# Kernel tuning notes

Hardware: AMD Instinct MI355X
Metric: run time of the kernel (lower is better)

Reference implementation:

```python
import jax, jax.numpy as jnp
import numpy as np

HIDDEN, FFN, N_EXPERTS, TOP_K = 1024, 4096, 8, 2


def setup_inputs() -> dict:
    key = jax.random.key(0)
    ks = jax.random.split(key, 8)
    s_h = 1.0 / np.sqrt(HIDDEN)
    s_f = 1.0 / np.sqrt(FFN)
    return {
        "x": jax.random.normal(ks[0], (1, 1024, HIDDEN), dtype=jnp.float32),
        "gate_w": jax.random.normal(ks[1], (N_EXPERTS, HIDDEN), dtype=jnp.float32) * s_h,
        "gate_b": jnp.zeros((N_EXPERTS,), dtype=jnp.float32),
        "w1": jax.random.normal(ks[2], (N_EXPERTS, HIDDEN, FFN), dtype=jnp.float32) * s_h,
        "b1": jnp.zeros((N_EXPERTS, FFN), dtype=jnp.float32),
        "w2": jax.random.normal(ks[3], (N_EXPERTS, FFN, HIDDEN), dtype=jnp.float32) * s_f,
        "b2": jnp.zeros((N_EXPERTS, HIDDEN), dtype=jnp.float32),
    }


def reference(x, gate_w, gate_b, w1, b1, w2, b2):
    B, S, H = x.shape
    x_flat = x.reshape(-1, H)  # (T, H)
    # Router: top-k gating with softmax over selected logits
    logits = x_flat @ gate_w.T + gate_b  # (T, E)
    top_w, sel = jax.lax.top_k(logits, TOP_K)  # (T, K)
    rw = jax.nn.softmax(top_w, axis=-1)  # (T, K)
    # combine[t, e] = router weight of expert e for token t (0 if not selected)
    combine = jnp.sum(jax.nn.one_hot(sel, N_EXPERTS, dtype=x.dtype) * rw[..., None], axis=1)  # (T, E)
    # Dense all-expert FFN, combined with routing weights (zero weight => zero contribution,
    # identical math to the masked gather/scatter loop in the torch module)
    h = jax.nn.gelu(jnp.einsum('th,ehf->tef', x_flat, w1) + b1, approximate=False)  # (T, E, F)
    y = jnp.einsum('tef,efh->teh', h, w2) + b2  # (T, E, H)
    out = jnp.einsum('te,teh->th', combine, y)  # (T, H)
    return out.reshape(B, S, H)
```

## Files before the change

### kernel.cpp

```cpp
#include <hip/hip_runtime.h>


typedef __bf16 bf16;
typedef __bf16 bf16x8 __attribute__((ext_vector_type(8)));
typedef float floatx4 __attribute__((ext_vector_type(4)));

#define T_TOK 1024
#define HID 1024
#define FFN 4096
#define NEXP 8
#define BM 128
#define BN 128
#define BK 32
#define LP 36

__global__ void xconv_k(const float* __restrict__ x, bf16* __restrict__ xb) {
  int i = blockIdx.x * 256 + threadIdx.x;
  float4 a = ((const float4*)x)[i * 2];
  float4 b = ((const float4*)x)[i * 2 + 1];
  bf16 t[8] = {(bf16)a.x, (bf16)a.y, (bf16)a.z, (bf16)a.w,
               (bf16)b.x, (bf16)b.y, (bf16)b.z, (bf16)b.w};
  *(bf16x8*)&xb[(size_t)i * 8] = *(bf16x8*)t;
}

__global__ void router_k(const float* __restrict__ x, const float* __restrict__ gw,
                         const float* __restrict__ gb, int* __restrict__ cnt,
                         int* __restrict__ elist, float* __restrict__ ewt) {
  int wave = threadIdx.x >> 6;
  int lane = threadIdx.x & 63;
  int t = blockIdx.x * 4 + wave;
  const float* xr = x + (size_t)t * HID;
  float xv[16];
#pragma unroll
  for (int j = 0; j < 16; j++) xv[j] = xr[lane + 64 * j];
  float logits[NEXP];
#pragma unroll
  for (int e = 0; e < NEXP; e++) {
    const float* g = gw + (size_t)e * HID;
    float s = 0.f;
#pragma unroll
    for (int j = 0; j < 16; j++) s += xv[j] * g[lane + 64 * j];
#pragma unroll
    for (int off = 32; off; off >>= 1) s += __shfl_xor(s, off, 64);
    logits[e] = s + gb[e];
  }
  int i0 = 0; float l0 = logits[0];
#pragma unroll
  for (int e = 1; e < NEXP; e++) if (logits[e] > l0) { l0 = logits[e]; i0 = e; }
  int i1 = -1; float l1 = -3.0e38f;
#pragma unroll
  for (int e = 0; e < NEXP; e++) if (e != i0 && logits[e] > l1) { l1 = logits[e]; i1 = e; }
  if (lane == 0) {
    float w0 = 1.f / (1.f + expf(l1 - l0));
    float w1 = 1.f - w0;
    int p0 = atomicAdd(cnt + i0, 1);
    elist[i0 * T_TOK + p0] = t * 2 + 0; ewt[i0 * T_TOK + p0] = w0;
    int p1 = atomicAdd(cnt + i1, 1);
    elist[i1 * T_TOK + p1] = t * 2 + 1; ewt[i1 * T_TOK + p1] = w1;
  }
}

__global__ __launch_bounds__(256)
void gemm1_k(const bf16* __restrict__ xb, const float* __restrict__ w1,
             const float* __restrict__ b1, const int* __restrict__ cnt,
             const int* __restrict__ elist, bf16* __restrict__ hbuf) {
  int e = blockIdx.z;
  int c = cnt[e];
  int m0 = blockIdx.y * BM;
  if (m0 >= c) return;
  int n0 = blockIdx.x * BN;

  __shared__ __align__(16) bf16 As[BM][LP];
  __shared__ __align__(16) bf16 Bs[BN][LP];

  int tid = threadIdx.x;
  int ar = tid >> 1;
  int ac = (tid & 1) * 16;
  int ra = m0 + ar; if (ra >= c) ra = c - 1;
  const bf16* aptr = xb + (size_t)(elist[e * T_TOK + ra] >> 1) * HID + ac;
  int bn = tid & 127;
  int bk = (tid >> 7) * 16;
  const float* bptr = w1 + (size_t)e * HID * FFN + (size_t)bk * FFN + n0 + bn;

  uint4 a0, a1;
  float bfl[16];
  a0 = *(const uint4*)(aptr);
  a1 = *(const uint4*)(aptr + 8);
#pragma unroll
  for (int j = 0; j < 16; j++) bfl[j] = bptr[(size_t)j * FFN];

  floatx4 acc[4][4] = {};
  int ln = tid & 63, wv = tid >> 6;
  int fm = ln & 15, quad = ln >> 4;
  int wm = (wv & 1) * 64, wn = (wv >> 1) * 64;

  for (int t = 0; t < HID / BK; t++) {
    bf16 bb[16];
#pragma unroll
    for (int j = 0; j < 16; j++) bb[j] = (bf16)bfl[j];
    uint4 wa0 = a0, wa1 = a1;
    __syncthreads();
    *(uint4*)&As[ar][ac]      = wa0;
    *(uint4*)&As[ar][ac + 8]  = wa1;
    *(bf16x8*)&Bs[bn][bk]     = *(bf16x8*)&bb[0];
    *(bf16x8*)&Bs[bn][bk + 8] = *(bf16x8*)&bb[8];
    if (t + 1 < HID / BK) {
      aptr += BK;
      a0 = *(const uint4*)(aptr);
      a1 = *(const uint4*)(aptr + 8);
      bptr += (size_t)BK * FFN;
#pragma unroll
      for (int j = 0; j < 16; j++) bfl[j] = bptr[(size_t)j * FFN];
    }
    __syncthreads();
    bf16x8 af[4], bfr[4];
#pragma unroll
    for (int i = 0; i < 4; i++) af[i] = *(const bf16x8*)&As[wm + i * 16 + fm][quad * 8];
#pragma unroll
    for (int j = 0; j < 4; j++) bfr[j] = *(const bf16x8*)&Bs[wn + j * 16 + fm][quad * 8];
#pragma unroll
    for (int i = 0; i < 4; i++)
#pragma unroll
      for (int j = 0; j < 4; j++)
        acc[i][j] = __builtin_amdgcn_mfma_f32_16x16x32_bf16(af[i], bfr[j], acc[i][j], 0, 0, 0);
  }

  const float* b1e = b1 + (size_t)e * FFN;
#pragma unroll
  for (int i = 0; i < 4; i++) {
    int rb = m0 + wm + i * 16 + quad * 4;
#pragma unroll
    for (int j = 0; j < 4; j++) {
      int col = n0 + wn + j * 16 + fm;
      float bias = b1e[col];
#pragma unroll
      for (int r = 0; r < 4; r++) {
        int row = rb + r;
        if (row < c) {
          int slot = elist[e * T_TOK + row];
          float v = acc[i][j][r] + bias;
          float g = 0.5f * v * (1.f + erff(v * 0.70710678118654752f));
          hbuf[(size_t)slot * FFN + col] = (bf16)g;
        }
      }
    }
  }
}

__global__ __launch_bounds__(256)
void gemm2_k(const bf16* __restrict__ hbuf, const float* __restrict__ w2,
             const float* __restrict__ b2, const int* __restrict__ cnt,
             const int* __restrict__ elist, const float* __restrict__ ewt,
             float* __restrict__ part) {
  int e = blockIdx.z & 7;
  int ks = blockIdx.z >> 3;
  int c = cnt[e];
  int m0 = blockIdx.y * BM;
  if (m0 >= c) return;
  int n0 = blockIdx.x * BN;
  int kbeg = ks * (FFN / 4);

  __shared__ __align__(16) bf16 As[BM][LP];
  __shared__ __align__(16) bf16 Bs[BN][LP];

  int tid = threadIdx.x;
  int ar = tid >> 1;
  int ac = (tid & 1) * 16;
  int ra = m0 + ar; if (ra >= c) ra = c - 1;
  const bf16* aptr = hbuf + (size_t)elist[e * T_TOK + ra] * FFN + kbeg + ac;
  int bn = tid & 127;
  int bk = (tid >> 7) * 16;
  const float* bptr = w2 + (size_t)e * FFN * HID + (size_t)(kbeg + bk) * HID + n0 + bn;

  uint4 a0, a1;
  float bfl[16];
  a0 = *(const uint4*)(aptr);
  a1 = *(const uint4*)(aptr + 8);
#pragma unroll
  for (int j = 0; j < 16; j++) bfl[j] = bptr[(size_t)j * HID];

  floatx4 acc[4][4] = {};
  int ln = tid & 63, wv = tid >> 6;
  int fm = ln & 15, quad = ln >> 4;
  int wm = (wv & 1) * 64, wn = (wv >> 1) * 64;

  const int NT = (FFN / 4) / BK;
  for (int t = 0; t < NT; t++) {
    bf16 bb[16];
#pragma unroll
    for (int j = 0; j < 16; j++) bb[j] = (bf16)bfl[j];
    uint4 wa0 = a0, wa1 = a1;
    __syncthreads();
    *(uint4*)&As[ar][ac]      = wa0;
    *(uint4*)&As[ar][ac + 8]  = wa1;
    *(bf16x8*)&Bs[bn][bk]     = *(bf16x8*)&bb[0];
    *(bf16x8*)&Bs[bn][bk + 8] = *(bf16x8*)&bb[8];
    if (t + 1 < NT) {
      aptr += BK;
      a0 = *(const uint4*)(aptr);
      a1 = *(const uint4*)(aptr + 8);
      bptr += (size_t)BK * HID;
#pragma unroll
      for (int j = 0; j < 16; j++) bfl[j] = bptr[(size_t)j * HID];
    }
    __syncthreads();
    bf16x8 af[4], bfr[4];
#pragma unroll
    for (int i = 0; i < 4; i++) af[i] = *(const bf16x8*)&As[wm + i * 16 + fm][quad * 8];
#pragma unroll
    for (int j = 0; j < 4; j++) bfr[j] = *(const bf16x8*)&Bs[wn + j * 16 + fm][quad * 8];
#pragma unroll
    for (int i = 0; i < 4; i++)
#pragma unroll
      for (int j = 0; j < 4; j++)
        acc[i][j] = __builtin_amdgcn_mfma_f32_16x16x32_bf16(af[i], bfr[j], acc[i][j], 0, 0, 0);
  }

  const float* b2e = b2 + (size_t)e * HID;
#pragma unroll
  for (int i = 0; i < 4; i++) {
    int rb = m0 + wm + i * 16 + quad * 4;
#pragma unroll
    for (int j = 0; j < 4; j++) {
      int col = n0 + wn + j * 16 + fm;
      float bias = (ks == 0) ? b2e[col] : 0.f;
#pragma unroll
      for (int r = 0; r < 4; r++) {
        int row = rb + r;
        if (row < c) {
          int slot = elist[e * T_TOK + row];
          float w = ewt[e * T_TOK + row];
          part[((size_t)ks * (2 * T_TOK) + slot) * HID + col] = w * (acc[i][j][r] + bias);
        }
      }
    }
  }
}

__global__ void combine_k(const float* __restrict__ part, float* __restrict__ out) {
  int i = blockIdx.x * 256 + threadIdx.x;
  int t = i >> 8;
  int h4 = (i & 255) * 4;
  float4 s = {0.f, 0.f, 0.f, 0.f};
#pragma unroll
  for (int ks = 0; ks < 4; ks++)
#pragma unroll
    for (int sl = 0; sl < 2; sl++) {
      float4 v = *(const float4*)&part[((size_t)ks * (2 * T_TOK) + t * 2 + sl) * HID + h4];
      s.x += v.x; s.y += v.y; s.z += v.z; s.w += v.w;
    }
  *(float4*)&out[(size_t)t * HID + h4] = s;
}

extern "C" void kernel_launch(void* const* d_in, const int* in_sizes, int n_in,
                              void* d_out, int out_size, void* d_ws, size_t ws_size,
                              hipStream_t stream) {
  const float* x  = (const float*)d_in[0];
  const float* gw = (const float*)d_in[1];
  const float* gb = (const float*)d_in[2];
  const float* w1 = (const float*)d_in[3];
  const float* b1 = (const float*)d_in[4];
  const float* w2 = (const float*)d_in[5];
  const float* b2 = (const float*)d_in[6];
  float* out = (float*)d_out;

  char* ws = (char*)d_ws;
  int*   cnt   = (int*)ws;
  int*   elist = (int*)(ws + 1024);
  float* ewt   = (float*)(ws + 1024 + 32768);
  bf16*  xb    = (bf16*)(ws + (1 << 16));
  bf16*  hbuf  = (bf16*)(ws + ((size_t)4 << 20));
  float* part  = (float*)(ws + ((size_t)24 << 20));

  hipMemsetAsync(cnt, 0, 32, stream);
  xconv_k<<<512, 256, 0, stream>>>(x, xb);
  router_k<<<T_TOK / 4, 256, 0, stream>>>(x, gw, gb, cnt, elist, ewt);
  gemm1_k<<<dim3(FFN / BN, 8, NEXP), 256, 0, stream>>>(xb, w1, b1, cnt, elist, hbuf);
  gemm2_k<<<dim3(HID / BN, 8, NEXP * 4), 256, 0, stream>>>(hbuf, w2, b2, cnt, elist, ewt, part);
  combine_k<<<(T_TOK * HID / 4) / 256, 256, 0, stream>>>(part, out);
}
```

Before: 436.2 us.

## Fuse x conversion into router, double-buffer GEMM loads, widen split-K

Folds the fp32-to-bf16 conversion of x into the router kernel and vectorises the router's loads, which removes one launch. Both expert GEMMs now prefetch two K-tiles ahead into register double buffers, load weights as float2 pairs, and pad the LDS rows from 36 to 40 elements. The second GEMM's split-K factor goes from 4 to 8 to put more blocks in flight. The price is more register pressure and twice as many partial buffers for the combine kernel to read.

```diff
diff --git a/kernel.cpp b/kernel.cpp
--- a/kernel.cpp
+++ b/kernel.cpp
@@ -12,34 +12,39 @@
 #define BM 128
 #define BN 128
 #define BK 32
-#define LP 36
-
-__global__ void xconv_k(const float* __restrict__ x, bf16* __restrict__ xb) {
-  int i = blockIdx.x * 256 + threadIdx.x;
-  float4 a = ((const float4*)x)[i * 2];
-  float4 b = ((const float4*)x)[i * 2 + 1];
-  bf16 t[8] = {(bf16)a.x, (bf16)a.y, (bf16)a.z, (bf16)a.w,
-               (bf16)b.x, (bf16)b.y, (bf16)b.z, (bf16)b.w};
-  *(bf16x8*)&xb[(size_t)i * 8] = *(bf16x8*)t;
-}
+#define LP 40
+#define KS2 8
 
 __global__ void router_k(const float* __restrict__ x, const float* __restrict__ gw,
                          const float* __restrict__ gb, int* __restrict__ cnt,
-                         int* __restrict__ elist, float* __restrict__ ewt) {
+                         int* __restrict__ elist, float* __restrict__ ewt,
+                         bf16* __restrict__ xb) {
   int wave = threadIdx.x >> 6;
   int lane = threadIdx.x & 63;
   int t = blockIdx.x * 4 + wave;
-  const float* xr = x + (size_t)t * HID;
-  float xv[16];
-#pragma unroll
-  for (int j = 0; j < 16; j++) xv[j] = xr[lane + 64 * j];
+  const float* xr = x + (size_t)t * HID + lane * 16;
+  float4 xv[4];
+#pragma unroll
+  for (int c = 0; c < 4; c++) xv[c] = ((const float4*)xr)[c];
+  bf16 tv[16];
+#pragma unroll
+  for (int c = 0; c < 4; c++) {
+    tv[c * 4 + 0] = (bf16)xv[c].x; tv[c * 4 + 1] = (bf16)xv[c].y;
+    tv[c * 4 + 2] = (bf16)xv[c].z; tv[c * 4 + 3] = (bf16)xv[c].w;
+  }
+  *(uint4*)&xb[(size_t)t * HID + lane * 16]     = ((uint4*)tv)[0];
+  *(uint4*)&xb[(size_t)t * HID + lane * 16 + 8] = ((uint4*)tv)[1];
+
   float logits[NEXP];
 #pragma unroll
   for (int e = 0; e < NEXP; e++) {
-    const float* g = gw + (size_t)e * HID;
+    const float* g = gw + (size_t)e * HID + lane * 16;
     float s = 0.f;
 #pragma unroll
-    for (int j = 0; j < 16; j++) s += xv[j] * g[lane + 64 * j];
+    for (int c = 0; c < 4; c++) {
+      float4 gv = ((const float4*)g)[c];
+      s += xv[c].x * gv.x + xv[c].y * gv.y + xv[c].z * gv.z + xv[c].w * gv.w;
+    }
 #pragma unroll
     for (int off = 32; off; off >>= 1) s += __shfl_xor(s, off, 64);
     logits[e] = s + gb[e];
@@ -74,56 +79,57 @@
   __shared__ __align__(16) bf16 Bs[BN][LP];
 
   int tid = threadIdx.x;
-  int ar = tid >> 1;
-  int ac = (tid & 1) * 16;
+  int ar = tid >> 1, ah = (tid & 1) * 16;
   int ra = m0 + ar; if (ra >= c) ra = c - 1;
-  const bf16* aptr = xb + (size_t)(elist[e * T_TOK + ra] >> 1) * HID + ac;
-  int bn = tid & 127;
-  int bk = (tid >> 7) * 16;
-  const float* bptr = w1 + (size_t)e * HID * FFN + (size_t)bk * FFN + n0 + bn;
-
-  uint4 a0, a1;
-  float bfl[16];
-  a0 = *(const uint4*)(aptr);
-  a1 = *(const uint4*)(aptr + 8);
-#pragma unroll
-  for (int j = 0; j < 16; j++) bfl[j] = bptr[(size_t)j * FFN];
+  const bf16* abase = xb + (size_t)(elist[e * T_TOK + ra] >> 1) * HID + ah;
+  int bn2 = (tid & 63) * 2;
+  int bq8 = (tid >> 6) * 8;
+  const float* bbase = w1 + (size_t)e * HID * FFN + (size_t)bq8 * FFN + n0 + bn2;
+
+  uint4 pa[2][2];
+  float2 pb[2][8];
+
+#define G1LOAD(s, kt) do { \
+    const bf16* ap = abase + (kt) * BK; \
+    pa[s][0] = *(const uint4*)ap; \
+    pa[s][1] = *(const uint4*)(ap + 8); \
+    const float* bp = bbase + (size_t)(kt) * BK * FFN; \
+    _Pragma("unroll") for (int j = 0; j < 8; j++) \
+      pb[s][j] = *(const float2*)(bp + (size_t)j * FFN); \
+  } while (0)
+
+  G1LOAD(0, 0);
+  G1LOAD(1, 1);
 
   floatx4 acc[4][4] = {};
   int ln = tid & 63, wv = tid >> 6;
   int fm = ln & 15, quad = ln >> 4;
   int wm = (wv & 1) * 64, wn = (wv >> 1) * 64;
-
-  for (int t = 0; t < HID / BK; t++) {
-    bf16 bb[16];
-#pragma unroll
-    for (int j = 0; j < 16; j++) bb[j] = (bf16)bfl[j];
-    uint4 wa0 = a0, wa1 = a1;
-    __syncthreads();
-    *(uint4*)&As[ar][ac]      = wa0;
-    *(uint4*)&As[ar][ac + 8]  = wa1;
-    *(bf16x8*)&Bs[bn][bk]     = *(bf16x8*)&bb[0];
-    *(bf16x8*)&Bs[bn][bk + 8] = *(bf16x8*)&bb[8];
-    if (t + 1 < HID / BK) {
-      aptr += BK;
-      a0 = *(const uint4*)(aptr);
-      a1 = *(const uint4*)(aptr + 8);
-      bptr += (size_t)BK * FFN;
-#pragma unroll
-      for (int j = 0; j < 16; j++) bfl[j] = bptr[(size_t)j * FFN];
-    }
-    __syncthreads();
-    bf16x8 af[4], bfr[4];
-#pragma unroll
-    for (int i = 0; i < 4; i++) af[i] = *(const bf16x8*)&As[wm + i * 16 + fm][quad * 8];
-#pragma unroll
-    for (int j = 0; j < 4; j++) bfr[j] = *(const bf16x8*)&Bs[wn + j * 16 + fm][quad * 8];
-#pragma unroll
-    for (int i = 0; i < 4; i++)
-#pragma unroll
-      for (int j = 0; j < 4; j++)
-        acc[i][j] = __builtin_amdgcn_mfma_f32_16x16x32_bf16(af[i], bfr[j], acc[i][j], 0, 0, 0);
-  }
+  const int NT = HID / BK;
+
+#define G1STEP(s, t) do { \
+    bf16 c0[8], c1[8]; \
+    _Pragma("unroll") for (int j = 0; j < 8; j++) { \
+      c0[j] = (bf16)pb[s][j].x; c1[j] = (bf16)pb[s][j].y; } \
+    uint4 wa0 = pa[s][0], wa1 = pa[s][1]; \
+    __syncthreads(); \
+    *(uint4*)&As[ar][ah]     = wa0; \
+    *(uint4*)&As[ar][ah + 8] = wa1; \
+    *(bf16x8*)&Bs[bn2][bq8]     = *(bf16x8*)c0; \
+    *(bf16x8*)&Bs[bn2 + 1][bq8] = *(bf16x8*)c1; \
+    if ((t) + 2 < NT) G1LOAD(s, (t) + 2); \
+    __syncthreads(); \
+    bf16x8 af[4], bfr[4]; \
+    _Pragma("unroll") for (int i = 0; i < 4; i++) \
+      af[i] = *(const bf16x8*)&As[wm + i * 16 + fm][quad * 8]; \
+    _Pragma("unroll") for (int j = 0; j < 4; j++) \
+      bfr[j] = *(const bf16x8*)&Bs[wn + j * 16 + fm][quad * 8]; \
+    _Pragma("unroll") for (int i = 0; i < 4; i++) \
+      _Pragma("unroll") for (int j = 0; j < 4; j++) \
+        acc[i][j] = __builtin_amdgcn_mfma_f32_16x16x32_bf16(af[i], bfr[j], acc[i][j], 0, 0, 0); \
+  } while (0)
+
+  for (int tt = 0; tt < NT; tt += 2) { G1STEP(0, tt); G1STEP(1, tt + 1); }
 
   const float* b1e = b1 + (size_t)e * FFN;
 #pragma unroll
@@ -158,63 +164,63 @@
   int m0 = blockIdx.y * BM;
   if (m0 >= c) return;
   int n0 = blockIdx.x * BN;
-  int kbeg = ks * (FFN / 4);
+  int kbeg = ks * (FFN / KS2);
 
   __shared__ __align__(16) bf16 As[BM][LP];
   __shared__ __align__(16) bf16 Bs[BN][LP];
 
   int tid = threadIdx.x;
-  int ar = tid >> 1;
-  int ac = (tid & 1) * 16;
+  int ar = tid >> 1, ah = (tid & 1) * 16;
   int ra = m0 + ar; if (ra >= c) ra = c - 1;
-  const bf16* aptr = hbuf + (size_t)elist[e * T_TOK + ra] * FFN + kbeg + ac;
-  int bn = tid & 127;
-  int bk = (tid >> 7) * 16;
-  const float* bptr = w2 + (size_t)e * FFN * HID + (size_t)(kbeg + bk) * HID + n0 + bn;
-
-  uint4 a0, a1;
-  float bfl[16];
-  a0 = *(const uint4*)(aptr);
-  a1 = *(const uint4*)(aptr + 8);
-#pragma unroll
-  for (int j = 0; j < 16; j++) bfl[j] = bptr[(size_t)j * HID];
+  const bf16* abase = hbuf + (size_t)elist[e * T_TOK + ra] * FFN + kbeg + ah;
+  int bn2 = (tid & 63) * 2;
+  int bq8 = (tid >> 6) * 8;
+  const float* bbase = w2 + (size_t)e * FFN * HID + (size_t)(kbeg + bq8) * HID + n0 + bn2;
+
+  uint4 pa[2][2];
+  float2 pb[2][8];
+
+#define G2LOAD(s, kt) do { \
+    const bf16* ap = abase + (kt) * BK; \
+    pa[s][0] = *(const uint4*)ap; \
+    pa[s][1] = *(const uint4*)(ap + 8); \
+    const float* bp = bbase + (size_t)(kt) * BK * HID; \
+    _Pragma("unroll") for (int j = 0; j < 8; j++) \
+      pb[s][j] = *(const float2*)(bp + (size_t)j * HID); \
+  } while (0)
+
+  G2LOAD(0, 0);
+  G2LOAD(1, 1);
 
   floatx4 acc[4][4] = {};
   int ln = tid & 63, wv = tid >> 6;
   int fm = ln & 15, quad = ln >> 4;
   int wm = (wv & 1) * 64, wn = (wv >> 1) * 64;
-
-  const int NT = (FFN / 4) / BK;
-  for (int t = 0; t < NT; t++) {
-    bf16 bb[16];
-#pragma unroll
-    for (int j = 0; j < 16; j++) bb[j] = (bf16)bfl[j];
-    uint4 wa0 = a0, wa1 = a1;
-    __syncthreads();
-    *(uint4*)&As[ar][ac]      = wa0;
-    *(uint4*)&As[ar][ac + 8]  = wa1;
-    *(bf16x8*)&Bs[bn][bk]     = *(bf16x8*)&bb[0];
-    *(bf16x8*)&Bs[bn][bk + 8] = *(bf16x8*)&bb[8];
-    if (t + 1 < NT) {
-      aptr += BK;
-      a0 = *(const uint4*)(aptr);
-      a1 = *(const uint4*)(aptr + 8);
-      bptr += (size_t)BK * HID;
-#pragma unroll
-      for (int j = 0; j < 16; j++) bfl[j] = bptr[(size_t)j * HID];
-    }
-    __syncthreads();
-    bf16x8 af[4], bfr[4];
-#pragma unroll
-    for (int i = 0; i < 4; i++) af[i] = *(const bf16x8*)&As[wm + i * 16 + fm][quad * 8];
-#pragma unroll
-    for (int j = 0; j < 4; j++) bfr[j] = *(const bf16x8*)&Bs[wn + j * 16 + fm][quad * 8];
-#pragma unroll
-    for (int i = 0; i < 4; i++)
-#pragma unroll
-      for (int j = 0; j < 4; j++)
-        acc[i][j] = __builtin_amdgcn_mfma_f32_16x16x32_bf16(af[i], bfr[j], acc[i][j], 0, 0, 0);
-  }
+  const int NT = (FFN / KS2) / BK;
+
+#define G2STEP(s, t) do { \
+    bf16 c0[8], c1[8]; \
+    _Pragma("unroll") for (int j = 0; j < 8; j++) { \
+      c0[j] = (bf16)pb[s][j].x; c1[j] = (bf16)pb[s][j].y; } \
+    uint4 wa0 = pa[s][0], wa1 = pa[s][1]; \
+    __syncthreads(); \
+    *(uint4*)&As[ar][ah]     = wa0; \
+    *(uint4*)&As[ar][ah + 8] = wa1; \
+    *(bf16x8*)&Bs[bn2][bq8]     = *(bf16x8*)c0; \
+    *(bf16x8*)&Bs[bn2 + 1][bq8] = *(bf16x8*)c1; \
+    if ((t) + 2 < NT) G2LOAD(s, (t) + 2); \
+    __syncthreads(); \
+    bf16x8 af[4], bfr[4]; \
+    _Pragma("unroll") for (int i = 0; i < 4; i++) \
+      af[i] = *(const bf16x8*)&As[wm + i * 16 + fm][quad * 8]; \
+    _Pragma("unroll") for (int j = 0; j < 4; j++) \
+      bfr[j] = *(const bf16x8*)&Bs[wn + j * 16 + fm][quad * 8]; \
+    _Pragma("unroll") for (int i = 0; i < 4; i++) \
+      _Pragma("unroll") for (int j = 0; j < 4; j++) \
+        acc[i][j] = __builtin_amdgcn_mfma_f32_16x16x32_bf16(af[i], bfr[j], acc[i][j], 0, 0, 0); \
+  } while (0)
+
+  for (int tt = 0; tt < NT; tt += 2) { G2STEP(0, tt); G2STEP(1, tt + 1); }
 
   const float* b2e = b2 + (size_t)e * HID;
 #pragma unroll
@@ -243,7 +249,7 @@
   int h4 = (i & 255) * 4;
   float4 s = {0.f, 0.f, 0.f, 0.f};
 #pragma unroll
-  for (int ks = 0; ks < 4; ks++)
+  for (int ks = 0; ks < KS2; ks++)
 #pragma unroll
     for (int sl = 0; sl < 2; sl++) {
       float4 v = *(const float4*)&part[((size_t)ks * (2 * T_TOK) + t * 2 + sl) * HID + h4];
@@ -273,9 +279,8 @@
   float* part  = (float*)(ws + ((size_t)24 << 20));
 
   hipMemsetAsync(cnt, 0, 32, stream);
-  xconv_k<<<512, 256, 0, stream>>>(x, xb);
-  router_k<<<T_TOK / 4, 256, 0, stream>>>(x, gw, gb, cnt, elist, ewt);
+  router_k<<<T_TOK / 4, 256, 0, stream>>>(x, gw, gb, cnt, elist, ewt, xb);
   gemm1_k<<<dim3(FFN / BN, 8, NEXP), 256, 0, stream>>>(xb, w1, b1, cnt, elist, hbuf);
-  gemm2_k<<<dim3(HID / BN, 8, NEXP * 4), 256, 0, stream>>>(hbuf, w2, b2, cnt, elist, ewt, part);
+  gemm2_k<<<dim3(HID / BN, 8, NEXP * KS2), 256, 0, stream>>>(hbuf, w2, b2, cnt, elist, ewt, part);
   combine_k<<<(T_TOK * HID / 4) / 256, 256, 0, stream>>>(part, out);
 }
```

Result: slower. 490.5 us (+12.4%).
